# Performance work log

Measured on AMD Instinct MI355X. Metric: run time of the kernel, lower is better.

The kernel has to match this reference:

```python
import jax, jax.numpy as jnp
import numpy as np

B, C, H = 128, 3, 224
PATCH_NUM, PS = 14, 16          # patch_size = image_size / patch_num
NP = PATCH_NUM * PATCH_NUM      # 196 patches
TOP_K = 20
D = 768                         # ViT-B hidden dim
NUM_CLASSES = 1000


def setup_inputs() -> dict:
    key = jax.random.key(0)
    k1, k2, k3, k4, k5 = jax.random.split(key, 5)
    return {
        "inputs": jax.random.normal(k1, (B, C, H, H), jnp.float32),
        "patch_grad": jax.random.normal(k2, (B, NP, D), jnp.float32),
        "attack_w": jax.random.uniform(k3, (C, H, H), jnp.float32),  # torch.rand init
        "w_cls": jax.random.normal(k4, (C * NP, NUM_CLASSES), jnp.float32) * 0.02,
        "targets": jax.random.randint(k5, (B,), 0, NUM_CLASSES),
    }


def reference(inputs, patch_grad, attack_w, w_cls, targets):
    # --- top-k patch selection from patch-embedding gradients ---
    # sum over batch, then over embedding dim -> [NP]
    sum_patch = patch_grad.sum(axis=0).sum(axis=1)
    _, top_idx = jax.lax.top_k(sum_patch, TOP_K)  # distinct patch indices

    # --- vectorized equivalent of the per-pixel double loop ---
    # patch (ix, iy) -> pixel block [ix*PS:(ix+1)*PS, iy*PS:(iy+1)*PS]
    ix = top_idx // PATCH_NUM
    iy = top_idx % PATCH_NUM
    mask_p = jnp.zeros((PATCH_NUM, PATCH_NUM), inputs.dtype).at[ix, iy].set(1.0)
    mask = jnp.kron(mask_p, jnp.ones((PS, PS), inputs.dtype))  # [H, H] pixel mask
    x = inputs + mask[None, None, :, :] * attack_w[None, :, :, :]  # [B,C,H,H]

    # --- surrogate classifier head (stand-in for aux_vit second forward) ---
    # per-patch average pool, flatten, linear -> logits [B, NUM_CLASSES]
    pooled = x.reshape(B, C, PATCH_NUM, PS, PATCH_NUM, PS).mean(axis=(3, 5))
    logits = pooled.reshape(B, -1) @ w_cls

    targets_prob = jax.nn.softmax(logits, axis=1)
    # original applies CrossEntropyLoss to the *probabilities* (treats them as logits)
    logp = jax.nn.log_softmax(targets_prob, axis=1)
    ce = -jnp.take_along_axis(logp, targets[:, None], axis=1)[:, 0]  # [B]

    u = 0.0
    l2loss = jnp.mean(attack_w * attack_w)
    loss = u * l2loss - (1.0 - u) * ce.mean()
    return targets_prob, loss
```

## Files before the change

### kernel.cpp

```cpp
#include <hip/hip_runtime.h>
#include <math.h>

#define PA_OFF    0
#define APOOL_OFF 25600
#define MA_OFF    26624
#define IPOOL_OFF 28672
#define PL_OFF    106496

__global__ __launch_bounds__(256) void k1a_pool(
    const float* __restrict__ inputs,
    const float* __restrict__ attack_w,
    float* __restrict__ ws)
{
  const int w    = blockIdx.x * 4 + (threadIdx.x >> 6);
  const int lane = threadIdx.x & 63;
  if (w >= 5418) return;
  const int img = w / 14, px = w - img * 14;
  const float* base = (img < 384)
      ? inputs + (size_t)img * 50176
      : attack_w + (size_t)(img - 384) * 50176;
  const float* src = base + px * 3584;

  float4 s = make_float4(0.f, 0.f, 0.f, 0.f);
  if (lane < 56) {
    float4 v[16];
    #pragma unroll
    for (int r = 0; r < 16; ++r)
      v[r] = *(const float4*)(src + r * 224 + lane * 4);
    #pragma unroll
    for (int r = 0; r < 16; ++r) {
      s.x += v[r].x; s.y += v[r].y; s.z += v[r].z; s.w += v[r].w;
    }
  }
  s.x += __shfl_xor(s.x, 1); s.y += __shfl_xor(s.y, 1);
  s.z += __shfl_xor(s.z, 1); s.w += __shfl_xor(s.w, 1);
  s.x += __shfl_xor(s.x, 2); s.y += __shfl_xor(s.y, 2);
  s.z += __shfl_xor(s.z, 2); s.w += __shfl_xor(s.w, 2);
  if ((lane & 3) == 0 && lane < 56) {
    const int py = lane >> 2;
    const float ps = ((s.x + s.y) + (s.z + s.w)) * (1.f / 256.f);
    if (img < 384) {
      const int b = img / 3, c = img - b * 3;
      ws[IPOOL_OFF + (size_t)b * 588 + c * 196 + px * 14 + py] = ps;
    } else {
      ws[APOOL_OFF + (img - 384) * 196 + px * 14 + py] = ps;
    }
  }
}

__global__ __launch_bounds__(256) void k1b_pgrad(
    const float* __restrict__ patch_grad,
    float* __restrict__ ws)
{
  const int w    = blockIdx.x * 4 + (threadIdx.x >> 6);
  const int lane = threadIdx.x & 63;
  const int R0   = w * 4;
  const float* base = patch_grad + (size_t)R0 * 768;

  float4 v[12];
  #pragma unroll
  for (int j = 0; j < 12; ++j)
    v[j] = *(const float4*)(base + (size_t)(lane + 64 * j) * 4);

  float s0 = 0.f, s1 = 0.f, s2 = 0.f, s3 = 0.f;
  #pragma unroll
  for (int j = 0; j < 3; ++j)  s0 += (v[j].x + v[j].y) + (v[j].z + v[j].w);
  #pragma unroll
  for (int j = 3; j < 6; ++j)  s1 += (v[j].x + v[j].y) + (v[j].z + v[j].w);
  #pragma unroll
  for (int j = 6; j < 9; ++j)  s2 += (v[j].x + v[j].y) + (v[j].z + v[j].w);
  #pragma unroll
  for (int j = 9; j < 12; ++j) s3 += (v[j].x + v[j].y) + (v[j].z + v[j].w);

  #pragma unroll
  for (int o = 32; o > 0; o >>= 1) {
    s0 += __shfl_down(s0, o, 64);
    s1 += __shfl_down(s1, o, 64);
    s2 += __shfl_down(s2, o, 64);
    s3 += __shfl_down(s3, o, 64);
  }
  if (lane == 0) {
    const int b = R0 / 196, p = R0 - b * 196;
    float* pa = ws + PA_OFF;
    pa[(p + 0) * 128 + b] = s0;
    pa[(p + 1) * 128 + b] = s1;
    pa[(p + 2) * 128 + b] = s2;
    pa[(p + 3) * 128 + b] = s3;
  }
}

__global__ __launch_bounds__(256) void k2_topk(float* __restrict__ ws,
                                               float* __restrict__ d_loss)
{
  __shared__ float sp[196];
  __shared__ float maskp[196];
  const int t = threadIdx.x;
  if (t < 196) {
    const float4* q = (const float4*)(ws + PA_OFF + (size_t)t * 128);
    float4 a = make_float4(0.f, 0.f, 0.f, 0.f);
    #pragma unroll
    for (int j = 0; j < 32; ++j) {
      const float4 v = q[j];
      a.x += v.x; a.y += v.y; a.z += v.z; a.w += v.w;
    }
    sp[t] = (a.x + a.y) + (a.z + a.w);
  }
  if (t == 0) *d_loss = 0.f;
  __syncthreads();
  if (t < 196) {
    const float v = sp[t];
    int cnt = 0;
    for (int j = 0; j < 196; ++j) {
      const float u = sp[j];
      cnt += (u > v || (u == v && j < t)) ? 1 : 0;
    }
    maskp[t] = (cnt < 20) ? 1.f : 0.f;
  }
  __syncthreads();
  for (int k = t; k < 588; k += 256) {
    const int p = k % 196;
    ws[MA_OFF + k] = maskp[p] * ws[APOOL_OFF + k];
  }
}

__global__ __launch_bounds__(256) void k3_gemm(const float* __restrict__ w_cls,
                                               float* __restrict__ ws)
{
  __shared__ __align__(16) float lp[147 * 8];
  const int bid = blockIdx.x;
  const int ks = bid & 3;
  const int nt = (bid >> 2) & 15;
  const int bg = bid >> 6;
  const int t  = threadIdx.x;
  const float* ipool = ws + IPOOL_OFF;
  const float* ma    = ws + MA_OFF;
  for (int idx = t; idx < 1176; idx += 256) {
    const int bb = idx / 147;
    const int kk = idx - bb * 147;
    const int k  = ks * 147 + kk;
    lp[kk * 8 + bb] = ipool[(size_t)(bg * 8 + bb) * 588 + k] + ma[k];
  }
  __syncthreads();
  const int lane = t & 63, g = t >> 6;
  const int n = nt * 64 + lane;
  const bool valid = n < 1000;
  float a0 = 0, a1 = 0;
  const float* wc = w_cls + (size_t)ks * 147 * 1000 + n;
  #pragma unroll 7
  for (int kk = 0; kk < 147; ++kk) {
    const float w = valid ? wc[(size_t)kk * 1000] : 0.f;
    const float2 pv = *(const float2*)&lp[kk * 8 + g * 2];
    a0 += pv.x * w; a1 += pv.y * w;
  }
  float* pl = ws + PL_OFF;
  const int rowb = ks * 128 + bg * 8 + g * 2;
  pl[(size_t)(rowb + 0) * 1024 + n] = a0;
  pl[(size_t)(rowb + 1) * 1024 + n] = a1;
}

__global__ __launch_bounds__(256) void k4_softmax(const float* __restrict__ ws,
                                                  const int* __restrict__ targets,
                                                  float* __restrict__ out)
{
  __shared__ float red[4];
  __shared__ float sh_pt;
  const int b = blockIdx.x, t = threadIdx.x;
  const float* pl = ws + PL_OFF;
  float l[4]; bool val[4];
  #pragma unroll
  for (int j = 0; j < 4; ++j) {
    const int n = j * 256 + t;
    val[j] = (n < 1000);
    float s = -INFINITY;
    if (val[j]) {
      s = 0.f;
      #pragma unroll
      for (int ks = 0; ks < 4; ++ks) s += pl[(size_t)(ks * 128 + b) * 1024 + n];
    }
    l[j] = s;
  }
  float m = fmaxf(fmaxf(l[0], l[1]), fmaxf(l[2], l[3]));
  #pragma unroll
  for (int o = 32; o > 0; o >>= 1) m = fmaxf(m, __shfl_down(m, o, 64));
  if ((t & 63) == 0) red[t >> 6] = m;
  __syncthreads();
  const float m1 = fmaxf(fmaxf(red[0], red[1]), fmaxf(red[2], red[3]));
  __syncthreads();
  float e[4]; float s = 0.f;
  #pragma unroll
  for (int j = 0; j < 4; ++j) { e[j] = val[j] ? expf(l[j] - m1) : 0.f; s += e[j]; }
  #pragma unroll
  for (int o = 32; o > 0; o >>= 1) s += __shfl_down(s, o, 64);
  if ((t & 63) == 0) red[t >> 6] = s;
  __syncthreads();
  const float S1 = red[0] + red[1] + red[2] + red[3];
  __syncthreads();
  const float inv = 1.f / S1;
  const int tgt = targets[b];
  float p[4];
  #pragma unroll
  for (int j = 0; j < 4; ++j) {
    const int n = j * 256 + t;
    if (val[j]) {
      p[j] = e[j] * inv;
      out[(size_t)b * 1000 + n] = p[j];
      if (n == tgt) sh_pt = p[j];
    } else {
      p[j] = -INFINITY;
    }
  }
  float m2 = fmaxf(fmaxf(p[0], p[1]), fmaxf(p[2], p[3]));
  #pragma unroll
  for (int o = 32; o > 0; o >>= 1) m2 = fmaxf(m2, __shfl_down(m2, o, 64));
  if ((t & 63) == 0) red[t >> 6] = m2;
  __syncthreads();
  const float M2 = fmaxf(fmaxf(red[0], red[1]), fmaxf(red[2], red[3]));
  __syncthreads();
  float s2 = 0.f;
  #pragma unroll
  for (int j = 0; j < 4; ++j) s2 += val[j] ? expf(p[j] - M2) : 0.f;
  #pragma unroll
  for (int o = 32; o > 0; o >>= 1) s2 += __shfl_down(s2, o, 64);
  if ((t & 63) == 0) red[t >> 6] = s2;
  __syncthreads();
  if (t == 0) {
    const float S2 = red[0] + red[1] + red[2] + red[3];
    const float lse2 = M2 + logf(S2);
    atomicAdd(out + 128000, (sh_pt - lse2) * (1.f / 128.f));
  }
}

extern "C" void kernel_launch(void* const* d_in, const int* in_sizes, int n_in,
                              void* d_out, int out_size, void* d_ws, size_t ws_size,
                              hipStream_t stream) {
  const float* inputs     = (const float*)d_in[0];
  const float* patch_grad = (const float*)d_in[1];
  const float* attack_w   = (const float*)d_in[2];
  const float* w_cls      = (const float*)d_in[3];
  const int*   targets    = (const int*)d_in[4];
  float* out = (float*)d_out;
  float* ws  = (float*)d_ws;

  hipLaunchKernelGGL(k1a_pool,  dim3(1355), dim3(256), 0, stream, inputs, attack_w, ws);
  hipLaunchKernelGGL(k1b_pgrad, dim3(1568), dim3(256), 0, stream, patch_grad, ws);
  hipLaunchKernelGGL(k2_topk,   dim3(1),    dim3(256), 0, stream, ws, out + 128000);
  hipLaunchKernelGGL(k3_gemm,   dim3(1024), dim3(256), 0, stream, w_cls, ws);
  hipLaunchKernelGGL(k4_softmax, dim3(128), dim3(256), 0, stream, ws, targets, out);
}
```

Measured before the change: 212.4 us.

## Fuse pooling and patch-grad reduction kernels into one launch with staged loads

```diff
diff --git a/kernel.cpp b/kernel.cpp
--- a/kernel.cpp
+++ b/kernel.cpp
@@ -7,85 +7,97 @@
 #define IPOOL_OFF 28672
 #define PL_OFF    106496
 
-__global__ __launch_bounds__(256) void k1a_pool(
+__device__ __forceinline__ float hsum(float4 v) { return (v.x + v.y) + (v.z + v.w); }
+
+__global__ __launch_bounds__(256, 4) void k1_main(
     const float* __restrict__ inputs,
+    const float* __restrict__ patch_grad,
     const float* __restrict__ attack_w,
     float* __restrict__ ws)
 {
-  const int w    = blockIdx.x * 4 + (threadIdx.x >> 6);
+  const int bid  = blockIdx.x;
   const int lane = threadIdx.x & 63;
-  if (w >= 5418) return;
-  const int img = w / 14, px = w - img * 14;
-  const float* base = (img < 384)
-      ? inputs + (size_t)img * 50176
-      : attack_w + (size_t)(img - 384) * 50176;
-  const float* src = base + px * 3584;
-
-  float4 s = make_float4(0.f, 0.f, 0.f, 0.f);
-  if (lane < 56) {
-    float4 v[16];
-    #pragma unroll
-    for (int r = 0; r < 16; ++r)
-      v[r] = *(const float4*)(src + r * 224 + lane * 4);
-    #pragma unroll
-    for (int r = 0; r < 16; ++r) {
-      s.x += v[r].x; s.y += v[r].y; s.z += v[r].z; s.w += v[r].w;
-    }
-  }
-  s.x += __shfl_xor(s.x, 1); s.y += __shfl_xor(s.y, 1);
-  s.z += __shfl_xor(s.z, 1); s.w += __shfl_xor(s.w, 1);
-  s.x += __shfl_xor(s.x, 2); s.y += __shfl_xor(s.y, 2);
-  s.z += __shfl_xor(s.z, 2); s.w += __shfl_xor(s.w, 2);
-  if ((lane & 3) == 0 && lane < 56) {
-    const int py = lane >> 2;
-    const float ps = ((s.x + s.y) + (s.z + s.w)) * (1.f / 256.f);
-    if (img < 384) {
-      const int b = img / 3, c = img - b * 3;
-      ws[IPOOL_OFF + (size_t)b * 588 + c * 196 + px * 14 + py] = ps;
-    } else {
-      ws[APOOL_OFF + (img - 384) * 196 + px * 14 + py] = ps;
-    }
-  }
-}
-
-__global__ __launch_bounds__(256) void k1b_pgrad(
-    const float* __restrict__ patch_grad,
-    float* __restrict__ ws)
-{
-  const int w    = blockIdx.x * 4 + (threadIdx.x >> 6);
-  const int lane = threadIdx.x & 63;
-  const int R0   = w * 4;
-  const float* base = patch_grad + (size_t)R0 * 768;
-
-  float4 v[12];
-  #pragma unroll
-  for (int j = 0; j < 12; ++j)
-    v[j] = *(const float4*)(base + (size_t)(lane + 64 * j) * 4);
-
-  float s0 = 0.f, s1 = 0.f, s2 = 0.f, s3 = 0.f;
-  #pragma unroll
-  for (int j = 0; j < 3; ++j)  s0 += (v[j].x + v[j].y) + (v[j].z + v[j].w);
-  #pragma unroll
-  for (int j = 3; j < 6; ++j)  s1 += (v[j].x + v[j].y) + (v[j].z + v[j].w);
-  #pragma unroll
-  for (int j = 6; j < 9; ++j)  s2 += (v[j].x + v[j].y) + (v[j].z + v[j].w);
-  #pragma unroll
-  for (int j = 9; j < 12; ++j) s3 += (v[j].x + v[j].y) + (v[j].z + v[j].w);
-
-  #pragma unroll
-  for (int o = 32; o > 0; o >>= 1) {
-    s0 += __shfl_down(s0, o, 64);
-    s1 += __shfl_down(s1, o, 64);
-    s2 += __shfl_down(s2, o, 64);
-    s3 += __shfl_down(s3, o, 64);
-  }
-  if (lane == 0) {
-    const int b = R0 / 196, p = R0 - b * 196;
-    float* pa = ws + PA_OFF;
-    pa[(p + 0) * 128 + b] = s0;
-    pa[(p + 1) * 128 + b] = s1;
-    pa[(p + 2) * 128 + b] = s2;
-    pa[(p + 3) * 128 + b] = s3;
+
+  if (bid < 784) {
+    const int w  = bid * 4 + (threadIdx.x >> 6);
+    const int R0 = w * 8;
+    const float4* src = (const float4*)patch_grad + (size_t)R0 * 192 + lane;
+
+    float4 va[6], vb[6];
+    #pragma unroll
+    for (int j = 0; j < 6; ++j) va[j] = src[(size_t)j * 64];
+    __builtin_amdgcn_sched_barrier(0);
+    #pragma unroll
+    for (int j = 0; j < 6; ++j) vb[j] = src[(size_t)(6 + j) * 64];
+    __builtin_amdgcn_sched_barrier(0);
+
+    float s[8];
+    s[0] = hsum(va[0]) + hsum(va[1]) + hsum(va[2]);
+    s[1] = hsum(va[3]) + hsum(va[4]) + hsum(va[5]);
+    #pragma unroll
+    for (int j = 0; j < 6; ++j) va[j] = src[(size_t)(12 + j) * 64];
+    __builtin_amdgcn_sched_barrier(0);
+    s[2] = hsum(vb[0]) + hsum(vb[1]) + hsum(vb[2]);
+    s[3] = hsum(vb[3]) + hsum(vb[4]) + hsum(vb[5]);
+    #pragma unroll
+    for (int j = 0; j < 6; ++j) vb[j] = src[(size_t)(18 + j) * 64];
+    __builtin_amdgcn_sched_barrier(0);
+    s[4] = hsum(va[0]) + hsum(va[1]) + hsum(va[2]);
+    s[5] = hsum(va[3]) + hsum(va[4]) + hsum(va[5]);
+    s[6] = hsum(vb[0]) + hsum(vb[1]) + hsum(vb[2]);
+    s[7] = hsum(vb[3]) + hsum(vb[4]) + hsum(vb[5]);
+
+    #pragma unroll
+    for (int o = 32; o > 0; o >>= 1) {
+      #pragma unroll
+      for (int k = 0; k < 8; ++k) s[k] += __shfl_down(s[k], o, 64);
+    }
+    if (lane == 0) {
+      float* pa = ws + PA_OFF;
+      #pragma unroll
+      for (int k = 0; k < 8; ++k) {
+        const int row = R0 + k, b = row / 196, p = row - b * 196;
+        pa[p * 128 + b] = s[k];
+      }
+    }
+  } else {
+    const int w = (bid - 784) * 4 + (threadIdx.x >> 6);
+    if (w >= 5418) return;
+    const int img = w / 14, px = w - img * 14;
+    const float* base = (img < 384)
+        ? inputs + (size_t)img * 50176
+        : attack_w + (size_t)(img - 384) * 50176;
+    const float* src = base + px * 3584;
+    const int cl = (lane < 56) ? lane : 55;
+
+    float4 v[8], u[8];
+    #pragma unroll
+    for (int r = 0; r < 8; ++r) v[r] = *(const float4*)(src + r * 224 + cl * 4);
+    __builtin_amdgcn_sched_barrier(0);
+    #pragma unroll
+    for (int r = 0; r < 8; ++r) u[r] = *(const float4*)(src + (8 + r) * 224 + cl * 4);
+    __builtin_amdgcn_sched_barrier(0);
+
+    float4 s = make_float4(0.f, 0.f, 0.f, 0.f);
+    #pragma unroll
+    for (int r = 0; r < 8; ++r) {
+      s.x += v[r].x + u[r].x; s.y += v[r].y + u[r].y;
+      s.z += v[r].z + u[r].z; s.w += v[r].w + u[r].w;
+    }
+    s.x += __shfl_xor(s.x, 1); s.y += __shfl_xor(s.y, 1);
+    s.z += __shfl_xor(s.z, 1); s.w += __shfl_xor(s.w, 1);
+    s.x += __shfl_xor(s.x, 2); s.y += __shfl_xor(s.y, 2);
+    s.z += __shfl_xor(s.z, 2); s.w += __shfl_xor(s.w, 2);
+    if ((lane & 3) == 0 && lane < 56) {
+      const int py = lane >> 2;
+      const float ps = ((s.x + s.y) + (s.z + s.w)) * (1.f / 256.f);
+      if (img < 384) {
+        const int b = img / 3, c = img - b * 3;
+        ws[IPOOL_OFF + (size_t)b * 588 + c * 196 + px * 14 + py] = ps;
+      } else {
+        ws[APOOL_OFF + (img - 384) * 196 + px * 14 + py] = ps;
+      }
+    }
   }
 }
 
@@ -146,7 +158,7 @@
   const bool valid = n < 1000;
   float a0 = 0, a1 = 0;
   const float* wc = w_cls + (size_t)ks * 147 * 1000 + n;
-  #pragma unroll 7
+  #pragma unroll 21
   for (int kk = 0; kk < 147; ++kk) {
     const float w = valid ? wc[(size_t)kk * 1000] : 0.f;
     const float2 pv = *(const float2*)&lp[kk * 8 + g * 2];
@@ -241,9 +253,9 @@
   float* out = (float*)d_out;
   float* ws  = (float*)d_ws;
 
-  hipLaunchKernelGGL(k1a_pool,  dim3(1355), dim3(256), 0, stream, inputs, attack_w, ws);
-  hipLaunchKernelGGL(k1b_pgrad, dim3(1568), dim3(256), 0, stream, patch_grad, ws);
-  hipLaunchKernelGGL(k2_topk,   dim3(1),    dim3(256), 0, stream, ws, out + 128000);
-  hipLaunchKernelGGL(k3_gemm,   dim3(1024), dim3(256), 0, stream, w_cls, ws);
+  hipLaunchKernelGGL(k1_main,  dim3(2139), dim3(256), 0, stream,
+                     inputs, patch_grad, attack_w, ws);
+  hipLaunchKernelGGL(k2_topk,  dim3(1),    dim3(256), 0, stream, ws, out + 128000);
+  hipLaunchKernelGGL(k3_gemm,  dim3(1024), dim3(256), 0, stream, w_cls, ws);
   hipLaunchKernelGGL(k4_softmax, dim3(128), dim3(256), 0, stream, ws, targets, out);
 }
```

Result: faster. 205.3 us (-3.3%).
